# Optimization experiments

Hardware: AMD Instinct MI355X
Metric: run time of the kernel (lower is better)

Reference implementation:

```python
import jax, jax.numpy as jnp
import numpy as np

B, S, D, H = 4, 1024, 1024, 16
DH = D // H  # head dim = 64
NEG = 1e9  # keras Softmax masking constant for fp32


def setup_inputs() -> dict:
    key = jax.random.key(0)
    ks = jax.random.split(key, 7)
    return {
        "inputs": jax.random.normal(ks[0], (B, S, D), jnp.float32),
        "mask": jax.random.randint(ks[1], (B, 1, 1, S), 0, 2) > 0,
        "interaction": jax.random.normal(ks[2], (B, S, S, H), jnp.float32) * 0.1,
        "W_Q": jax.random.normal(ks[3], (D, D), jnp.float32) * 0.02,
        "W_K": jax.random.normal(ks[4], (D, D), jnp.float32) * 0.02,
        "W_V": jax.random.normal(ks[5], (D, D), jnp.float32) * 0.02,
        "W_O": jax.random.normal(ks[6], (D, D), jnp.float32) * 0.02,
    }


def reference(inputs, mask, interaction, W_Q, W_K, W_V, W_O):
    b, s, d = inputs.shape
    def proj(W):
        # [B,S,D] @ [D,D] -> [B,S,H,DH] -> [B,H,S,DH]
        return (inputs @ W).reshape(b, s, H, DH).transpose(0, 2, 1, 3)
    Q, K, V = proj(W_Q), proj(W_K), proj(W_V)
    scores = jnp.einsum("bhqd,bhkd->bhqk", Q, K) / (DH ** 0.5)
    # interaction [B,S,S,H] -> [B,H,S,S], additive bias before softmax
    scores = scores + interaction.transpose(0, 3, 1, 2)
    # keras Softmax(mask=...): add -1e9 where mask is False, softmax over last axis
    scores = jnp.where(mask, scores, scores - NEG)
    attn = jax.nn.softmax(scores, axis=-1)
    hidden = jnp.einsum("bhqk,bhkd->bhqd", attn, V)
    hidden = hidden.transpose(0, 2, 1, 3).reshape(b, s, d)
    return hidden @ W_O
```

## Files before the change

### kernel.cpp

```cpp
#include <hip/hip_runtime.h>
#include <hip/hip_bf16.h>
#include <stdint.h>

#define BDIM 4
#define SDIM 1024
#define DDIM 1024
#define HDIM 16
#define DHDIM 64

typedef __bf16 bf16_t;
typedef __bf16 bf16x8 __attribute__((ext_vector_type(8)));
typedef __bf16 bf16x4 __attribute__((ext_vector_type(4)));
typedef float f32x4 __attribute__((ext_vector_type(4)));

typedef __attribute__((address_space(3))) uint32_t lds_u32;
typedef const __attribute__((address_space(1))) uint32_t glb_u32;

__device__ __forceinline__ void glds16(const void* g, void* l) {
    __builtin_amdgcn_global_load_lds((glb_u32*)g, (lds_u32*)l, 16, 0, 0);
}


__global__ __launch_bounds__(256) void convert_x_kernel(const float* __restrict__ X,
                                                        bf16_t* __restrict__ Xb, int n) {
    int i = (blockIdx.x * 256 + threadIdx.x) * 4;
    if (i >= n) return;
    float4 v = *(const float4*)(X + i);
    bf16x4 o;
    o[0] = (bf16_t)v.x; o[1] = (bf16_t)v.y; o[2] = (bf16_t)v.z; o[3] = (bf16_t)v.w;
    *(bf16x4*)(Xb + i) = o;
}

__global__ __launch_bounds__(256) void transpose_w_kernel(const float* __restrict__ W0,
                                                          const float* __restrict__ W1,
                                                          const float* __restrict__ W2,
                                                          const float* __restrict__ W3,
                                                          bf16_t* __restrict__ Wt) {
    __shared__ float tile[32][33];
    int z = blockIdx.z;
    const float* W = (z == 0) ? W0 : (z == 1) ? W1 : (z == 2) ? W2 : W3;
    bf16_t* dst = Wt + (size_t)z * DDIM * DDIM;
    int bx = blockIdx.x * 32;
    int by = blockIdx.y * 32;
    int x = threadIdx.x & 31, y0 = threadIdx.x >> 5;
#pragma unroll
    for (int i = 0; i < 4; i++) {
        int y = y0 + i * 8;
        tile[y][x] = W[(size_t)(by + y) * DDIM + bx + x];
    }
    __syncthreads();
#pragma unroll
    for (int i = 0; i < 4; i++) {
        int y = y0 + i * 8;
        dst[(size_t)(bx + y) * DDIM + by + x] = (bf16_t)tile[x][y];
    }
}

__global__ __launch_bounds__(1024) void mask_flag_kernel(const unsigned char* __restrict__ mb,
                                                         int* __restrict__ flag) {
    __shared__ int any;
    if (threadIdx.x == 0) any = 0;
    __syncthreads();
    int loc = 0;
    for (int i = threadIdx.x; i < BDIM * SDIM; i += 1024)
        if ((i & 3) && mb[i]) loc = 1;
    if (loc) any = 1;
    __syncthreads();
    if (threadIdx.x == 0) *flag = any ? 1 : 0;
}

template <int MODE>
__global__ __launch_bounds__(256) void gemm_bt_kernel(const bf16_t* __restrict__ A,
                                                      const bf16_t* __restrict__ Bt,
                                                      bf16_t* __restrict__ Qo, bf16_t* __restrict__ Ko,
                                                      bf16_t* __restrict__ Vto, float* __restrict__ Co) {
    __shared__ bf16_t As[128 * 32];
    __shared__ bf16_t Bs[128 * 32];
    const int m0 = blockIdx.x * 128;
    const int n0 = blockIdx.y * 128;
    const int t = threadIdx.x;
    const int lane = t & 63, w = t >> 6;
    const int wm = w & 1, wn = w >> 1;
    const int low = lane & 15, quad = lane >> 4;
    f32x4 acc[4][4] = {};

    const int srow = w * 16 + (lane >> 2);
    const int koff = (lane & 3) * 8;
    const bf16_t* Ag = A + (size_t)(m0 + srow) * DDIM + koff;
    const bf16_t* Bg = Bt + (size_t)(n0 + srow) * DDIM + koff;
    bf16_t* AsW = As + w * 512;
    bf16_t* BsW = Bs + w * 512;

    for (int k0 = 0; k0 < DDIM; k0 += 32) {
        __syncthreads();
        glds16(Ag + k0, AsW);
        glds16(Ag + (size_t)64 * DDIM + k0, AsW + 64 * 32);
        glds16(Bg + k0, BsW);
        glds16(Bg + (size_t)64 * DDIM + k0, BsW + 64 * 32);
        __syncthreads();
        bf16x8 af[4], bv[4];
#pragma unroll
        for (int mt = 0; mt < 4; mt++)
            af[mt] = *(const bf16x8*)(As + (wm * 64 + mt * 16 + low) * 32 + quad * 8);
#pragma unroll
        for (int nt = 0; nt < 4; nt++)
            bv[nt] = *(const bf16x8*)(Bs + (wn * 64 + nt * 16 + low) * 32 + quad * 8);
#pragma unroll
        for (int mt = 0; mt < 4; mt++)
#pragma unroll
            for (int nt = 0; nt < 4; nt++)
                acc[mt][nt] = __builtin_amdgcn_mfma_f32_16x16x32_bf16(af[mt], bv[nt], acc[mt][nt], 0, 0, 0);
    }

#pragma unroll
    for (int mt = 0; mt < 4; mt++) {
        const int mbase = m0 + wm * 64 + mt * 16 + quad * 4;
#pragma unroll
        for (int nt = 0; nt < 4; nt++) {
            const int ncol = n0 + wn * 64 + nt * 16 + low;
            if (MODE == 0) {
                const int which = ncol >> 10, nl = ncol & 1023;
                const int hh = nl >> 6, dh = nl & 63;
                const int bb = mbase >> 10, s = mbase & 1023;
                if (which == 2) {
                    bf16x4 pv;
#pragma unroll
                    for (int r = 0; r < 4; r++) pv[r] = (bf16_t)acc[mt][nt][r];
                    *(bf16x4*)(Vto + ((size_t)((bb * HDIM + hh) * DHDIM + dh)) * SDIM + s) = pv;
                } else if (which == 0) {
#pragma unroll
                    for (int r = 0; r < 4; r++)
                        Qo[((size_t)(bb * HDIM + hh) * SDIM + (s + r)) * DHDIM + dh] =
                            (bf16_t)(acc[mt][nt][r] * 0.125f);
                } else {
#pragma unroll
                    for (int r = 0; r < 4; r++)
                        Ko[((size_t)(bb * HDIM + hh) * SDIM + (s + r)) * DHDIM + dh] =
                            (bf16_t)acc[mt][nt][r];
                }
            } else {
#pragma unroll
                for (int r = 0; r < 4; r++)
                    Co[(size_t)(mbase + r) * DDIM + ncol] = acc[mt][nt][r];
            }
        }
    }
}

__global__ __launch_bounds__(1024, 4) void attn_kernel(const bf16_t* __restrict__ Q,
                                                       const bf16_t* __restrict__ K,
                                                       const bf16_t* __restrict__ Vt,
                                                       const float* __restrict__ inter,
                                                       const unsigned char* __restrict__ maskb,
                                                       const int* __restrict__ flagp,
                                                       bf16_t* __restrict__ hid) {
    constexpr int KS = 40;
    constexpr int HS = 16 * KS + 8;
    __shared__ bf16_t bias_l[2][16 * HS];
    __shared__ bf16_t P[16][16 * KS];
    const int b = blockIdx.y;
    const int q0 = blockIdx.x * 16;
    const int t = threadIdx.x;
    const int w = t >> 6, lane = t & 63;
    const int low = lane & 15, quad = lane >> 4;
    const int h = w;
    const int mstride = (*flagp) ? 1 : 4;

    const int sh = lane & 15;
    const int sk0 = (lane >> 4) * 8;
    const float* srcB = inter + ((size_t)(b * SDIM + q0 + w) * SDIM + sk0) * HDIM + sh;
    const unsigned char* mb = maskb + (size_t)b * SDIM * mstride;
    const int stoff = sh * HS + w * KS + sk0;

    const bf16_t* Qb = Q + ((size_t)(b * HDIM + h) * SDIM + q0) * DHDIM;
    bf16x8 qf0 = *(const bf16x8*)(Qb + low * DHDIM + quad * 8);
    bf16x8 qf1 = *(const bf16x8*)(Qb + low * DHDIM + 32 + quad * 8);

    const bf16_t* Kb = K + (size_t)(b * HDIM + h) * SDIM * DHDIM;
    const bf16_t* VtB = Vt + (size_t)(b * HDIM + h) * DHDIM * SDIM;
    bf16_t* Pw = &P[w][0];

    float mrow = -3.0e38f, lrow = 0.f;
    f32x4 accO[4] = {};

    bf16x8 kA0 = *(const bf16x8*)(Kb + (size_t)(0 + low) * DHDIM + quad * 8);
    bf16x8 kA1 = *(const bf16x8*)(Kb + (size_t)(0 + low) * DHDIM + 32 + quad * 8);
    bf16x8 kB0 = *(const bf16x8*)(Kb + (size_t)(16 + low) * DHDIM + quad * 8);
    bf16x8 kB1 = *(const bf16x8*)(Kb + (size_t)(16 + low) * DHDIM + 32 + quad * 8);
    {
        float b0v[8], pen0[8];
#pragma unroll
        for (int j = 0; j < 8; j++) b0v[j] = srcB[j * HDIM];
        if (mstride == 1) {
            uint64_t mw = *(const uint64_t*)(mb + sk0);
#pragma unroll
            for (int j = 0; j < 8; j++) pen0[j] = ((mw >> (8 * j)) & 0xff) ? 0.f : 1.0e9f;
        } else {
            const int4* mp = (const int4*)(mb + (size_t)sk0 * 4);
            int4 ma = mp[0], mc = mp[1];
            pen0[0] = ma.x ? 0.f : 1.0e9f; pen0[1] = ma.y ? 0.f : 1.0e9f;
            pen0[2] = ma.z ? 0.f : 1.0e9f; pen0[3] = ma.w ? 0.f : 1.0e9f;
            pen0[4] = mc.x ? 0.f : 1.0e9f; pen0[5] = mc.y ? 0.f : 1.0e9f;
            pen0[6] = mc.z ? 0.f : 1.0e9f; pen0[7] = mc.w ? 0.f : 1.0e9f;
        }
        bf16x8 bw;
#pragma unroll
        for (int j = 0; j < 8; j++) bw[j] = (bf16_t)(b0v[j] - pen0[j]);
        *(bf16x8*)(&bias_l[0][stoff]) = bw;
    }

    for (int c = 0; c < SDIM / 32; c++) {
        __syncthreads();
        const int kbase = c * 32;

        bf16x8 vf[4];
#pragma unroll
        for (int nt = 0; nt < 4; nt++)
            vf[nt] = *(const bf16x8*)(VtB + (size_t)(nt * 16 + low) * SDIM + kbase + quad * 8);

        bf16x8 nA0, nA1, nB0, nB1;
        float nb[8], npen[8];
        if (c < SDIM / 32 - 1) {
            const int k2 = kbase + 32;
            const bf16_t* kpA = Kb + (size_t)(k2 + low) * DHDIM;
            const bf16_t* kpB = Kb + (size_t)(k2 + 16 + low) * DHDIM;
            nA0 = *(const bf16x8*)(kpA + quad * 8);
            nA1 = *(const bf16x8*)(kpA + 32 + quad * 8);
            nB0 = *(const bf16x8*)(kpB + quad * 8);
            nB1 = *(const bf16x8*)(kpB + 32 + quad * 8);
            const float* s2 = srcB + (size_t)(c + 1) * 512;
#pragma unroll
            for (int j = 0; j < 8; j++) nb[j] = s2[j * HDIM];
            const int kb2 = k2 + sk0;
            if (mstride == 1) {
                uint64_t mw = *(const uint64_t*)(mb + kb2);
#pragma unroll
                for (int j = 0; j < 8; j++) npen[j] = ((mw >> (8 * j)) & 0xff) ? 0.f : 1.0e9f;
            } else {
                const int4* mp = (const int4*)(mb + (size_t)kb2 * 4);
                int4 ma = mp[0], mc = mp[1];
                npen[0] = ma.x ? 0.f : 1.0e9f; npen[1] = ma.y ? 0.f : 1.0e9f;
                npen[2] = ma.z ? 0.f : 1.0e9f; npen[3] = ma.w ? 0.f : 1.0e9f;
                npen[4] = mc.x ? 0.f : 1.0e9f; npen[5] = mc.y ? 0.f : 1.0e9f;
                npen[6] = mc.z ? 0.f : 1.0e9f; npen[7] = mc.w ? 0.f : 1.0e9f;
            }
        }

        f32x4 s0 = {}, s1 = {};
        s0 = __builtin_amdgcn_mfma_f32_16x16x32_bf16(kA0, qf0, s0, 0, 0, 0);
        s0 = __builtin_amdgcn_mfma_f32_16x16x32_bf16(kA1, qf1, s0, 0, 0, 0);
        s1 = __builtin_amdgcn_mfma_f32_16x16x32_bf16(kB0, qf0, s1, 0, 0, 0);
        s1 = __builtin_amdgcn_mfma_f32_16x16x32_bf16(kB1, qf1, s1, 0, 0, 0);

        const bf16_t* bc = &bias_l[c & 1][h * HS + low * KS];
        bf16x4 bv0 = *(const bf16x4*)(bc + quad * 4);
        bf16x4 bv1 = *(const bf16x4*)(bc + 16 + quad * 4);
        float sv[8];
#pragma unroll
        for (int r = 0; r < 4; r++) {
            sv[r] = s0[r] + (float)bv0[r];
            sv[4 + r] = s1[r] + (float)bv1[r];
        }

        float vmx = sv[0];
#pragma unroll
        for (int j = 1; j < 8; j++) vmx = fmaxf(vmx, sv[j]);
        vmx = fmaxf(vmx, __shfl_xor(vmx, 16));
        vmx = fmaxf(vmx, __shfl_xor(vmx, 32));
        float mn = fmaxf(mrow, vmx);
        float alpha = __expf(mrow - mn);
        mrow = mn;
        float ps = 0.f;
        bf16x4 p0, p1;
#pragma unroll
        for (int j = 0; j < 4; j++) {
            float e0 = __expf(sv[j] - mn);
            float e1 = __expf(sv[4 + j] - mn);
            ps += e0 + e1;
            p0[j] = (bf16_t)e0;
            p1[j] = (bf16_t)e1;
        }
        ps += __shfl_xor(ps, 16);
        ps += __shfl_xor(ps, 32);
        lrow = lrow * alpha + ps;

#pragma unroll
        for (int r = 0; r < 4; r++) {
            float ar = __shfl(alpha, (lane & 48) | (quad * 4 + r));
#pragma unroll
            for (int nt = 0; nt < 4; nt++) accO[nt][r] *= ar;
        }

        *(bf16x4*)(Pw + low * KS + quad * 4) = p0;
        *(bf16x4*)(Pw + low * KS + 16 + quad * 4) = p1;
        bf16x8 pf = *(const bf16x8*)(Pw + low * KS + quad * 8);

#pragma unroll
        for (int nt = 0; nt < 4; nt++)
            accO[nt] = __builtin_amdgcn_mfma_f32_16x16x32_bf16(pf, vf[nt], accO[nt], 0, 0, 0);

        if (c < SDIM / 32 - 1) {
            bf16x8 bw;
#pragma unroll
            for (int j = 0; j < 8; j++) bw[j] = (bf16_t)(nb[j] - npen[j]);
            *(bf16x8*)(&bias_l[(c + 1) & 1][stoff]) = bw;
            kA0 = nA0; kA1 = nA1; kB0 = nB0; kB1 = nB1;
        }
    }

    float linv = 1.f / lrow;
#pragma unroll
    for (int r = 0; r < 4; r++) {
        float lr = __shfl(linv, (lane & 48) | (quad * 4 + r));
#pragma unroll
        for (int nt = 0; nt < 4; nt++) {
            hid[((size_t)b * SDIM + q0 + quad * 4 + r) * DDIM + h * 64 + nt * 16 + low] =
                (bf16_t)(accO[nt][r] * lr);
        }
    }
}


extern "C" void kernel_launch(void* const* d_in, const int* in_sizes, int n_in,
                              void* d_out, int out_size, void* d_ws, size_t ws_size,
                              hipStream_t stream) {
    const float* X = (const float*)d_in[0];
    const unsigned char* maskb = (const unsigned char*)d_in[1];
    const float* inter = (const float*)d_in[2];
    const float* WQ = (const float*)d_in[3];
    const float* WK = (const float*)d_in[4];
    const float* WV = (const float*)d_in[5];
    const float* WO = (const float*)d_in[6];
    float* out = (float*)d_out;

    char* ws = (char*)d_ws;
    const size_t MB = 1024 * 1024;
    bf16_t* Xb  = (bf16_t*)(ws + 0 * MB);
    bf16_t* Wt  = (bf16_t*)(ws + 8 * MB);
    bf16_t* Qm  = (bf16_t*)(ws + 16 * MB);
    bf16_t* Km  = (bf16_t*)(ws + 24 * MB);
    bf16_t* Vtm = (bf16_t*)(ws + 32 * MB);
    bf16_t* hid = (bf16_t*)(ws + 40 * MB);
    int* flag   = (int*)(ws + 48 * MB);

    convert_x_kernel<<<BDIM * SDIM * DDIM / (256 * 4), 256, 0, stream>>>(X, Xb, BDIM * SDIM * DDIM);
    transpose_w_kernel<<<dim3(32, 32, 4), 256, 0, stream>>>(WQ, WK, WV, WO, Wt);
    mask_flag_kernel<<<1, 1024, 0, stream>>>(maskb, flag);
    gemm_bt_kernel<0><<<dim3(32, 24), 256, 0, stream>>>(Xb, Wt, Qm, Km, Vtm, nullptr);
    attn_kernel<<<dim3(SDIM / 16, BDIM), 1024, 0, stream>>>(Qm, Km, Vtm, inter, maskb, flag, hid);
    gemm_bt_kernel<1><<<dim3(32, 8), 256, 0, stream>>>(hid, Wt + (size_t)3 * DDIM * DDIM,
                                                       nullptr, nullptr, nullptr, out);
}
```

Before: 543.0 us.

## Restructure attention blocks to 32 queries x 8 heads with XCD-aware mapping

The attention kernel now gives each block 32 query rows and half the heads (8 waves, 512 threads) instead of 16 rows and all 16 heads. Each K/V fragment is reused for two 16-row query tiles, and block IDs are mapped so blocks sharing a batch and head half land on the same XCD, which should improve L2 locality. The interaction bias is loaded as float4 vectors along the head axis with a scalar mask read, replacing strided scalar loads. The cost is that K prefetch into registers is dropped, the bias is written to LDS with scalar bf16 stores, the grid shrinks to 256 blocks, and register pressure rises from two sets of accumulators.

```diff
diff --git a/kernel.cpp b/kernel.cpp
--- a/kernel.cpp
+++ b/kernel.cpp
@@ -147,175 +147,212 @@
     }
 }
 
-__global__ __launch_bounds__(1024, 4) void attn_kernel(const bf16_t* __restrict__ Q,
-                                                       const bf16_t* __restrict__ K,
-                                                       const bf16_t* __restrict__ Vt,
-                                                       const float* __restrict__ inter,
-                                                       const unsigned char* __restrict__ maskb,
-                                                       const int* __restrict__ flagp,
-                                                       bf16_t* __restrict__ hid) {
+__global__ __launch_bounds__(512, 4) void attn_kernel(const bf16_t* __restrict__ Q,
+                                                      const bf16_t* __restrict__ K,
+                                                      const bf16_t* __restrict__ Vt,
+                                                      const float* __restrict__ inter,
+                                                      const unsigned char* __restrict__ maskb,
+                                                      const int* __restrict__ flagp,
+                                                      bf16_t* __restrict__ hid) {
     constexpr int KS = 40;
     constexpr int HS = 16 * KS + 8;
-    __shared__ bf16_t bias_l[2][16 * HS];
-    __shared__ bf16_t P[16][16 * KS];
-    const int b = blockIdx.y;
-    const int q0 = blockIdx.x * 16;
+    constexpr int BUFE = 2 * 8 * HS;
+    __shared__ bf16_t bias_l[2][BUFE];
+    __shared__ bf16_t P[8][16 * KS];
+    const int bid = blockIdx.x;
+    const int xcd = bid & 7;
+    const int b = xcd >> 1, hh = xcd & 1, qi = bid >> 3;
+    const int q0 = qi * 32;
     const int t = threadIdx.x;
     const int w = t >> 6, lane = t & 63;
     const int low = lane & 15, quad = lane >> 4;
-    const int h = w;
+    const int h = hh * 8 + w;
     const int mstride = (*flagp) ? 1 : 4;
 
-    const int sh = lane & 15;
-    const int sk0 = (lane >> 4) * 8;
-    const float* srcB = inter + ((size_t)(b * SDIM + q0 + w) * SDIM + sk0) * HDIM + sh;
+    const int sk = lane >> 1, shp = lane & 1;
+    const float* srcB = inter + ((size_t)(b * SDIM + q0) * SDIM + sk) * HDIM + hh * 8 + shp * 4;
     const unsigned char* mb = maskb + (size_t)b * SDIM * mstride;
-    const int stoff = sh * HS + w * KS + sk0;
+    constexpr size_t ROWSTRIDE = (size_t)SDIM * HDIM;
 
     const bf16_t* Qb = Q + ((size_t)(b * HDIM + h) * SDIM + q0) * DHDIM;
-    bf16x8 qf0 = *(const bf16x8*)(Qb + low * DHDIM + quad * 8);
-    bf16x8 qf1 = *(const bf16x8*)(Qb + low * DHDIM + 32 + quad * 8);
+    bf16x8 qa0 = *(const bf16x8*)(Qb + low * DHDIM + quad * 8);
+    bf16x8 qa1 = *(const bf16x8*)(Qb + low * DHDIM + 32 + quad * 8);
+    bf16x8 qb0 = *(const bf16x8*)(Qb + (16 + low) * DHDIM + quad * 8);
+    bf16x8 qb1 = *(const bf16x8*)(Qb + (16 + low) * DHDIM + 32 + quad * 8);
 
     const bf16_t* Kb = K + (size_t)(b * HDIM + h) * SDIM * DHDIM;
     const bf16_t* VtB = Vt + (size_t)(b * HDIM + h) * DHDIM * SDIM;
     bf16_t* Pw = &P[w][0];
 
-    float mrow = -3.0e38f, lrow = 0.f;
-    f32x4 accO[4] = {};
-
-    bf16x8 kA0 = *(const bf16x8*)(Kb + (size_t)(0 + low) * DHDIM + quad * 8);
-    bf16x8 kA1 = *(const bf16x8*)(Kb + (size_t)(0 + low) * DHDIM + 32 + quad * 8);
-    bf16x8 kB0 = *(const bf16x8*)(Kb + (size_t)(16 + low) * DHDIM + quad * 8);
-    bf16x8 kB1 = *(const bf16x8*)(Kb + (size_t)(16 + low) * DHDIM + 32 + quad * 8);
+    float mA = -3.0e38f, lA = 0.f, mB = -3.0e38f, lB = 0.f;
+    f32x4 accA[4] = {}, accB[4] = {};
+
     {
-        float b0v[8], pen0[8];
-#pragma unroll
-        for (int j = 0; j < 8; j++) b0v[j] = srcB[j * HDIM];
-        if (mstride == 1) {
-            uint64_t mw = *(const uint64_t*)(mb + sk0);
-#pragma unroll
-            for (int j = 0; j < 8; j++) pen0[j] = ((mw >> (8 * j)) & 0xff) ? 0.f : 1.0e9f;
-        } else {
-            const int4* mp = (const int4*)(mb + (size_t)sk0 * 4);
-            int4 ma = mp[0], mc = mp[1];
-            pen0[0] = ma.x ? 0.f : 1.0e9f; pen0[1] = ma.y ? 0.f : 1.0e9f;
-            pen0[2] = ma.z ? 0.f : 1.0e9f; pen0[3] = ma.w ? 0.f : 1.0e9f;
-            pen0[4] = mc.x ? 0.f : 1.0e9f; pen0[5] = mc.y ? 0.f : 1.0e9f;
-            pen0[6] = mc.z ? 0.f : 1.0e9f; pen0[7] = mc.w ? 0.f : 1.0e9f;
-        }
-        bf16x8 bw;
-#pragma unroll
-        for (int j = 0; j < 8; j++) bw[j] = (bf16_t)(b0v[j] - pen0[j]);
-        *(bf16x8*)(&bias_l[0][stoff]) = bw;
+        float4 v[4];
+#pragma unroll
+        for (int i = 0; i < 4; i++)
+            v[i] = *(const float4*)(srcB + (size_t)(w + i * 8) * ROWSTRIDE);
+        float pen = mb[sk * mstride] ? 0.f : 1.0e9f;
+#pragma unroll
+        for (int i = 0; i < 4; i++) {
+            const int r4 = w + i * 8;
+            bf16_t* d = &bias_l[0][(size_t)(r4 >> 4) * (8 * HS) + (shp * 4) * HS + (r4 & 15) * KS + sk];
+            d[0 * HS] = (bf16_t)(v[i].x - pen);
+            d[1 * HS] = (bf16_t)(v[i].y - pen);
+            d[2 * HS] = (bf16_t)(v[i].z - pen);
+            d[3 * HS] = (bf16_t)(v[i].w - pen);
+        }
     }
 
     for (int c = 0; c < SDIM / 32; c++) {
         __syncthreads();
         const int kbase = c * 32;
 
+        float4 nv[4]; float npen = 0.f;
+        if (c < SDIM / 32 - 1) {
+#pragma unroll
+            for (int i = 0; i < 4; i++)
+                nv[i] = *(const float4*)(srcB + (size_t)(w + i * 8) * ROWSTRIDE + (size_t)(c + 1) * 32 * HDIM);
+            npen = mb[((c + 1) * 32 + sk) * mstride] ? 0.f : 1.0e9f;
+        }
+
+        const bf16_t* kpA = Kb + (size_t)(kbase + low) * DHDIM;
+        const bf16_t* kpB = Kb + (size_t)(kbase + 16 + low) * DHDIM;
+        bf16x8 kA0 = *(const bf16x8*)(kpA + quad * 8);
+        bf16x8 kA1 = *(const bf16x8*)(kpA + 32 + quad * 8);
+        bf16x8 kB0 = *(const bf16x8*)(kpB + quad * 8);
+        bf16x8 kB1 = *(const bf16x8*)(kpB + 32 + quad * 8);
+
+        f32x4 sA0 = {}, sA1 = {}, sB0 = {}, sB1 = {};
+        sA0 = __builtin_amdgcn_mfma_f32_16x16x32_bf16(kA0, qa0, sA0, 0, 0, 0);
+        sA0 = __builtin_amdgcn_mfma_f32_16x16x32_bf16(kA1, qa1, sA0, 0, 0, 0);
+        sA1 = __builtin_amdgcn_mfma_f32_16x16x32_bf16(kB0, qa0, sA1, 0, 0, 0);
+        sA1 = __builtin_amdgcn_mfma_f32_16x16x32_bf16(kB1, qa1, sA1, 0, 0, 0);
+        sB0 = __builtin_amdgcn_mfma_f32_16x16x32_bf16(kA0, qb0, sB0, 0, 0, 0);
+        sB0 = __builtin_amdgcn_mfma_f32_16x16x32_bf16(kA1, qb1, sB0, 0, 0, 0);
+        sB1 = __builtin_amdgcn_mfma_f32_16x16x32_bf16(kB0, qb0, sB1, 0, 0, 0);
+        sB1 = __builtin_amdgcn_mfma_f32_16x16x32_bf16(kB1, qb1, sB1, 0, 0, 0);
+
         bf16x8 vf[4];
 #pragma unroll
         for (int nt = 0; nt < 4; nt++)
             vf[nt] = *(const bf16x8*)(VtB + (size_t)(nt * 16 + low) * SDIM + kbase + quad * 8);
 
-        bf16x8 nA0, nA1, nB0, nB1;
-        float nb[8], npen[8];
+        {
+            const bf16_t* bc = &bias_l[c & 1][(size_t)0 * (8 * HS) + w * HS + low * KS];
+            bf16x4 bv0 = *(const bf16x4*)(bc + quad * 4);
+            bf16x4 bv1 = *(const bf16x4*)(bc + 16 + quad * 4);
+            float sv[8];
+#pragma unroll
+            for (int r = 0; r < 4; r++) {
+                sv[r] = sA0[r] + (float)bv0[r];
+                sv[4 + r] = sA1[r] + (float)bv1[r];
+            }
+            float vmx = sv[0];
+#pragma unroll
+            for (int j = 1; j < 8; j++) vmx = fmaxf(vmx, sv[j]);
+            vmx = fmaxf(vmx, __shfl_xor(vmx, 16));
+            vmx = fmaxf(vmx, __shfl_xor(vmx, 32));
+            float mn = fmaxf(mA, vmx);
+            float alpha = __expf(mA - mn);
+            mA = mn;
+            float ps = 0.f;
+            bf16x4 p0, p1;
+#pragma unroll
+            for (int j = 0; j < 4; j++) {
+                float e0 = __expf(sv[j] - mn);
+                float e1 = __expf(sv[4 + j] - mn);
+                ps += e0 + e1;
+                p0[j] = (bf16_t)e0;
+                p1[j] = (bf16_t)e1;
+            }
+            ps += __shfl_xor(ps, 16);
+            ps += __shfl_xor(ps, 32);
+            lA = lA * alpha + ps;
+#pragma unroll
+            for (int r = 0; r < 4; r++) {
+                float ar = __shfl(alpha, (lane & 48) | (quad * 4 + r));
+#pragma unroll
+                for (int nt = 0; nt < 4; nt++) accA[nt][r] *= ar;
+            }
+            *(bf16x4*)(Pw + low * KS + quad * 4) = p0;
+            *(bf16x4*)(Pw + low * KS + 16 + quad * 4) = p1;
+            bf16x8 pf = *(const bf16x8*)(Pw + low * KS + quad * 8);
+#pragma unroll
+            for (int nt = 0; nt < 4; nt++)
+                accA[nt] = __builtin_amdgcn_mfma_f32_16x16x32_bf16(pf, vf[nt], accA[nt], 0, 0, 0);
+        }
+
+        {
+            const bf16_t* bc = &bias_l[c & 1][(size_t)1 * (8 * HS) + w * HS + low * KS];
+            bf16x4 bv0 = *(const bf16x4*)(bc + quad * 4);
+            bf16x4 bv1 = *(const bf16x4*)(bc + 16 + quad * 4);
+            float sv[8];
+#pragma unroll
+            for (int r = 0; r < 4; r++) {
+                sv[r] = sB0[r] + (float)bv0[r];
+                sv[4 + r] = sB1[r] + (float)bv1[r];
+            }
+            float vmx = sv[0];
+#pragma unroll
+            for (int j = 1; j < 8; j++) vmx = fmaxf(vmx, sv[j]);
+            vmx = fmaxf(vmx, __shfl_xor(vmx, 16));
+            vmx = fmaxf(vmx, __shfl_xor(vmx, 32));
+            float mn = fmaxf(mB, vmx);
+            float alpha = __expf(mB - mn);
+            mB = mn;
+            float ps = 0.f;
+            bf16x4 p0, p1;
+#pragma unroll
+            for (int j = 0; j < 4; j++) {
+                float e0 = __expf(sv[j] - mn);
+                float e1 = __expf(sv[4 + j] - mn);
+                ps += e0 + e1;
+                p0[j] = (bf16_t)e0;
+                p1[j] = (bf16_t)e1;
+            }
+            ps += __shfl_xor(ps, 16);
+            ps += __shfl_xor(ps, 32);
+            lB = lB * alpha + ps;
+#pragma unroll
+            for (int r = 0; r < 4; r++) {
+                float ar = __shfl(alpha, (lane & 48) | (quad * 4 + r));
+#pragma unroll
+                for (int nt = 0; nt < 4; nt++) accB[nt][r] *= ar;
+            }
+            *(bf16x4*)(Pw + low * KS + quad * 4) = p0;
+            *(bf16x4*)(Pw + low * KS + 16 + quad * 4) = p1;
+            bf16x8 pf = *(const bf16x8*)(Pw + low * KS + quad * 8);
+#pragma unroll
+            for (int nt = 0; nt < 4; nt++)
+                accB[nt] = __builtin_amdgcn_mfma_f32_16x16x32_bf16(pf, vf[nt], accB[nt], 0, 0, 0);
+        }
+
         if (c < SDIM / 32 - 1) {
-            const int k2 = kbase + 32;
-            const bf16_t* kpA = Kb + (size_t)(k2 + low) * DHDIM;
-            const bf16_t* kpB = Kb + (size_t)(k2 + 16 + low) * DHDIM;
-            nA0 = *(const bf16x8*)(kpA + quad * 8);
-            nA1 = *(const bf16x8*)(kpA + 32 + quad * 8);
-            nB0 = *(const bf16x8*)(kpB + quad * 8);
-            nB1 = *(const bf16x8*)(kpB + 32 + quad * 8);
-            const float* s2 = srcB + (size_t)(c + 1) * 512;
-#pragma unroll
-            for (int j = 0; j < 8; j++) nb[j] = s2[j * HDIM];
-            const int kb2 = k2 + sk0;
-            if (mstride == 1) {
-                uint64_t mw = *(const uint64_t*)(mb + kb2);
-#pragma unroll
-                for (int j = 0; j < 8; j++) npen[j] = ((mw >> (8 * j)) & 0xff) ? 0.f : 1.0e9f;
-            } else {
-                const int4* mp = (const int4*)(mb + (size_t)kb2 * 4);
-                int4 ma = mp[0], mc = mp[1];
-                npen[0] = ma.x ? 0.f : 1.0e9f; npen[1] = ma.y ? 0.f : 1.0e9f;
-                npen[2] = ma.z ? 0.f : 1.0e9f; npen[3] = ma.w ? 0.f : 1.0e9f;
-                npen[4] = mc.x ? 0.f : 1.0e9f; npen[5] = mc.y ? 0.f : 1.0e9f;
-                npen[6] = mc.z ? 0.f : 1.0e9f; npen[7] = mc.w ? 0.f : 1.0e9f;
-            }
-        }
-
-        f32x4 s0 = {}, s1 = {};
-        s0 = __builtin_amdgcn_mfma_f32_16x16x32_bf16(kA0, qf0, s0, 0, 0, 0);
-        s0 = __builtin_amdgcn_mfma_f32_16x16x32_bf16(kA1, qf1, s0, 0, 0, 0);
-        s1 = __builtin_amdgcn_mfma_f32_16x16x32_bf16(kB0, qf0, s1, 0, 0, 0);
-        s1 = __builtin_amdgcn_mfma_f32_16x16x32_bf16(kB1, qf1, s1, 0, 0, 0);
-
-        const bf16_t* bc = &bias_l[c & 1][h * HS + low * KS];
-        bf16x4 bv0 = *(const bf16x4*)(bc + quad * 4);
-        bf16x4 bv1 = *(const bf16x4*)(bc + 16 + quad * 4);
-        float sv[8];
-#pragma unroll
-        for (int r = 0; r < 4; r++) {
-            sv[r] = s0[r] + (float)bv0[r];
-            sv[4 + r] = s1[r] + (float)bv1[r];
-        }
-
-        float vmx = sv[0];
-#pragma unroll
-        for (int j = 1; j < 8; j++) vmx = fmaxf(vmx, sv[j]);
-        vmx = fmaxf(vmx, __shfl_xor(vmx, 16));
-        vmx = fmaxf(vmx, __shfl_xor(vmx, 32));
-        float mn = fmaxf(mrow, vmx);
-        float alpha = __expf(mrow - mn);
-        mrow = mn;
-        float ps = 0.f;
-        bf16x4 p0, p1;
-#pragma unroll
-        for (int j = 0; j < 4; j++) {
-            float e0 = __expf(sv[j] - mn);
-            float e1 = __expf(sv[4 + j] - mn);
-            ps += e0 + e1;
-            p0[j] = (bf16_t)e0;
-            p1[j] = (bf16_t)e1;
-        }
-        ps += __shfl_xor(ps, 16);
-        ps += __shfl_xor(ps, 32);
-        lrow = lrow * alpha + ps;
-
-#pragma unroll
-        for (int r = 0; r < 4; r++) {
-            float ar = __shfl(alpha, (lane & 48) | (quad * 4 + r));
-#pragma unroll
-            for (int nt = 0; nt < 4; nt++) accO[nt][r] *= ar;
-        }
-
-        *(bf16x4*)(Pw + low * KS + quad * 4) = p0;
-        *(bf16x4*)(Pw + low * KS + 16 + quad * 4) = p1;
-        bf16x8 pf = *(const bf16x8*)(Pw + low * KS + quad * 8);
-
-#pragma unroll
-        for (int nt = 0; nt < 4; nt++)
-            accO[nt] = __builtin_amdgcn_mfma_f32_16x16x32_bf16(pf, vf[nt], accO[nt], 0, 0, 0);
-
-        if (c < SDIM / 32 - 1) {
-            bf16x8 bw;
-#pragma unroll
-            for (int j = 0; j < 8; j++) bw[j] = (bf16_t)(nb[j] - npen[j]);
-            *(bf16x8*)(&bias_l[(c + 1) & 1][stoff]) = bw;
-            kA0 = nA0; kA1 = nA1; kB0 = nB0; kB1 = nB1;
-        }
-    }
-
-    float linv = 1.f / lrow;
+#pragma unroll
+            for (int i = 0; i < 4; i++) {
+                const int r4 = w + i * 8;
+                bf16_t* d = &bias_l[(c + 1) & 1]
+                                   [(size_t)(r4 >> 4) * (8 * HS) + (shp * 4) * HS + (r4 & 15) * KS + sk];
+                d[0 * HS] = (bf16_t)(nv[i].x - npen);
+                d[1 * HS] = (bf16_t)(nv[i].y - npen);
+                d[2 * HS] = (bf16_t)(nv[i].z - npen);
+                d[3 * HS] = (bf16_t)(nv[i].w - npen);
+            }
+        }
+    }
+
+    float liA = 1.f / lA, liB = 1.f / lB;
 #pragma unroll
     for (int r = 0; r < 4; r++) {
-        float lr = __shfl(linv, (lane & 48) | (quad * 4 + r));
+        float lrA = __shfl(liA, (lane & 48) | (quad * 4 + r));
+        float lrB = __shfl(liB, (lane & 48) | (quad * 4 + r));
 #pragma unroll
         for (int nt = 0; nt < 4; nt++) {
             hid[((size_t)b * SDIM + q0 + quad * 4 + r) * DDIM + h * 64 + nt * 16 + low] =
-                (bf16_t)(accO[nt][r] * lr);
+                (bf16_t)(accA[nt][r] * lrA);
+            hid[((size_t)b * SDIM + q0 + 16 + quad * 4 + r) * DDIM + h * 64 + nt * 16 + low] =
+                (bf16_t)(accB[nt][r] * lrB);
         }
     }
 }
@@ -347,7 +384,7 @@
     transpose_w_kernel<<<dim3(32, 32, 4), 256, 0, stream>>>(WQ, WK, WV, WO, Wt);
     mask_flag_kernel<<<1, 1024, 0, stream>>>(maskb, flag);
     gemm_bt_kernel<0><<<dim3(32, 24), 256, 0, stream>>>(Xb, Wt, Qm, Km, Vtm, nullptr);
-    attn_kernel<<<dim3(SDIM / 16, BDIM), 1024, 0, stream>>>(Qm, Km, Vtm, inter, maskb, flag, hid);
+    attn_kernel<<<dim3(256), 512, 0, stream>>>(Qm, Km, Vtm, inter, maskb, flag, hid);
     gemm_bt_kernel<1><<<dim3(32, 8), 256, 0, stream>>>(hid, Wt + (size_t)3 * DDIM * DDIM,
                                                        nullptr, nullptr, nullptr, out);
 }
```

Result: faster. 529.8 us (-2.4%).

## Split attention blocks per head-half with XCD-aware mapping and lazy softmax rescale

Applied to the files above, without the earlier changes.

The attention kernel now uses 512-thread blocks, each covering 8 heads instead of 16. Blocks are assigned through a 1D grid whose low bits pick the batch and head-half, so each XCD works on one (batch, head-half) pair and gets better L2 locality for K and V. The interaction bias is loaded with float4 reads along the head dimension and scattered into LDS as bf16. K fragments are no longer register-prefetched one chunk ahead. The online softmax skips rescaling unless the running max grows by more than 8, which cuts exp and multiply work but lets unnormalized values grow up to e^8 and adds a wave vote.

```diff
diff --git a/kernel.cpp b/kernel.cpp
--- a/kernel.cpp
+++ b/kernel.cpp
@@ -147,30 +147,31 @@
     }
 }
 
-__global__ __launch_bounds__(1024, 4) void attn_kernel(const bf16_t* __restrict__ Q,
-                                                       const bf16_t* __restrict__ K,
-                                                       const bf16_t* __restrict__ Vt,
-                                                       const float* __restrict__ inter,
-                                                       const unsigned char* __restrict__ maskb,
-                                                       const int* __restrict__ flagp,
-                                                       bf16_t* __restrict__ hid) {
+__global__ __launch_bounds__(512, 4) void attn_kernel(const bf16_t* __restrict__ Q,
+                                                      const bf16_t* __restrict__ K,
+                                                      const bf16_t* __restrict__ Vt,
+                                                      const float* __restrict__ inter,
+                                                      const unsigned char* __restrict__ maskb,
+                                                      const int* __restrict__ flagp,
+                                                      bf16_t* __restrict__ hid) {
     constexpr int KS = 40;
     constexpr int HS = 16 * KS + 8;
-    __shared__ bf16_t bias_l[2][16 * HS];
-    __shared__ bf16_t P[16][16 * KS];
-    const int b = blockIdx.y;
-    const int q0 = blockIdx.x * 16;
+    __shared__ bf16_t bias_l[2][8 * HS];
+    __shared__ bf16_t P[8][16 * KS];
+    const int bid = blockIdx.x;
+    const int xcd = bid & 7;
+    const int b = xcd >> 1, hh = xcd & 1;
+    const int q0 = (bid >> 3) * 16;
     const int t = threadIdx.x;
     const int w = t >> 6, lane = t & 63;
     const int low = lane & 15, quad = lane >> 4;
-    const int h = w;
+    const int h = hh * 8 + w;
     const int mstride = (*flagp) ? 1 : 4;
 
-    const int sh = lane & 15;
-    const int sk0 = (lane >> 4) * 8;
-    const float* srcB = inter + ((size_t)(b * SDIM + q0 + w) * SDIM + sk0) * HDIM + sh;
+    const int sk = lane >> 1, shp = lane & 1;
+    const float* srcB = inter + ((size_t)(b * SDIM + q0) * SDIM + sk) * HDIM + hh * 8 + shp * 4;
     const unsigned char* mb = maskb + (size_t)b * SDIM * mstride;
-    const int stoff = sh * HS + w * KS + sk0;
+    constexpr size_t ROWSTRIDE = (size_t)SDIM * HDIM;
 
     const bf16_t* Qb = Q + ((size_t)(b * HDIM + h) * SDIM + q0) * DHDIM;
     bf16x8 qf0 = *(const bf16x8*)(Qb + low * DHDIM + quad * 8);
@@ -183,67 +184,40 @@
     float mrow = -3.0e38f, lrow = 0.f;
     f32x4 accO[4] = {};
 
-    bf16x8 kA0 = *(const bf16x8*)(Kb + (size_t)(0 + low) * DHDIM + quad * 8);
-    bf16x8 kA1 = *(const bf16x8*)(Kb + (size_t)(0 + low) * DHDIM + 32 + quad * 8);
-    bf16x8 kB0 = *(const bf16x8*)(Kb + (size_t)(16 + low) * DHDIM + quad * 8);
-    bf16x8 kB1 = *(const bf16x8*)(Kb + (size_t)(16 + low) * DHDIM + 32 + quad * 8);
     {
-        float b0v[8], pen0[8];
-#pragma unroll
-        for (int j = 0; j < 8; j++) b0v[j] = srcB[j * HDIM];
-        if (mstride == 1) {
-            uint64_t mw = *(const uint64_t*)(mb + sk0);
-#pragma unroll
-            for (int j = 0; j < 8; j++) pen0[j] = ((mw >> (8 * j)) & 0xff) ? 0.f : 1.0e9f;
-        } else {
-            const int4* mp = (const int4*)(mb + (size_t)sk0 * 4);
-            int4 ma = mp[0], mc = mp[1];
-            pen0[0] = ma.x ? 0.f : 1.0e9f; pen0[1] = ma.y ? 0.f : 1.0e9f;
-            pen0[2] = ma.z ? 0.f : 1.0e9f; pen0[3] = ma.w ? 0.f : 1.0e9f;
-            pen0[4] = mc.x ? 0.f : 1.0e9f; pen0[5] = mc.y ? 0.f : 1.0e9f;
-            pen0[6] = mc.z ? 0.f : 1.0e9f; pen0[7] = mc.w ? 0.f : 1.0e9f;
-        }
-        bf16x8 bw;
-#pragma unroll
-        for (int j = 0; j < 8; j++) bw[j] = (bf16_t)(b0v[j] - pen0[j]);
-        *(bf16x8*)(&bias_l[0][stoff]) = bw;
+        float4 v0 = *(const float4*)(srcB + (size_t)w * ROWSTRIDE);
+        float4 v1 = *(const float4*)(srcB + (size_t)(w + 8) * ROWSTRIDE);
+        float pen = mb[sk * mstride] ? 0.f : 1.0e9f;
+        bf16_t* d0 = &bias_l[0][(shp * 4) * HS + w * KS + sk];
+        bf16_t* d1 = &bias_l[0][(shp * 4) * HS + (w + 8) * KS + sk];
+        d0[0 * HS] = (bf16_t)(v0.x - pen); d0[1 * HS] = (bf16_t)(v0.y - pen);
+        d0[2 * HS] = (bf16_t)(v0.z - pen); d0[3 * HS] = (bf16_t)(v0.w - pen);
+        d1[0 * HS] = (bf16_t)(v1.x - pen); d1[1 * HS] = (bf16_t)(v1.y - pen);
+        d1[2 * HS] = (bf16_t)(v1.z - pen); d1[3 * HS] = (bf16_t)(v1.w - pen);
     }
 
     for (int c = 0; c < SDIM / 32; c++) {
         __syncthreads();
         const int kbase = c * 32;
 
+        const bf16_t* kpA = Kb + (size_t)(kbase + low) * DHDIM;
+        const bf16_t* kpB = Kb + (size_t)(kbase + 16 + low) * DHDIM;
+        bf16x8 kA0 = *(const bf16x8*)(kpA + quad * 8);
+        bf16x8 kA1 = *(const bf16x8*)(kpA + 32 + quad * 8);
+        bf16x8 kB0 = *(const bf16x8*)(kpB + quad * 8);
+        bf16x8 kB1 = *(const bf16x8*)(kpB + 32 + quad * 8);
+
         bf16x8 vf[4];
 #pragma unroll
         for (int nt = 0; nt < 4; nt++)
             vf[nt] = *(const bf16x8*)(VtB + (size_t)(nt * 16 + low) * SDIM + kbase + quad * 8);
 
-        bf16x8 nA0, nA1, nB0, nB1;
-        float nb[8], npen[8];
+        float4 nv0, nv1; float npen = 0.f;
         if (c < SDIM / 32 - 1) {
-            const int k2 = kbase + 32;
-            const bf16_t* kpA = Kb + (size_t)(k2 + low) * DHDIM;
-            const bf16_t* kpB = Kb + (size_t)(k2 + 16 + low) * DHDIM;
-            nA0 = *(const bf16x8*)(kpA + quad * 8);
-            nA1 = *(const bf16x8*)(kpA + 32 + quad * 8);
-            nB0 = *(const bf16x8*)(kpB + quad * 8);
-            nB1 = *(const bf16x8*)(kpB + 32 + quad * 8);
-            const float* s2 = srcB + (size_t)(c + 1) * 512;
-#pragma unroll
-            for (int j = 0; j < 8; j++) nb[j] = s2[j * HDIM];
-            const int kb2 = k2 + sk0;
-            if (mstride == 1) {
-                uint64_t mw = *(const uint64_t*)(mb + kb2);
-#pragma unroll
-                for (int j = 0; j < 8; j++) npen[j] = ((mw >> (8 * j)) & 0xff) ? 0.f : 1.0e9f;
-            } else {
-                const int4* mp = (const int4*)(mb + (size_t)kb2 * 4);
-                int4 ma = mp[0], mc = mp[1];
-                npen[0] = ma.x ? 0.f : 1.0e9f; npen[1] = ma.y ? 0.f : 1.0e9f;
-                npen[2] = ma.z ? 0.f : 1.0e9f; npen[3] = ma.w ? 0.f : 1.0e9f;
-                npen[4] = mc.x ? 0.f : 1.0e9f; npen[5] = mc.y ? 0.f : 1.0e9f;
-                npen[6] = mc.z ? 0.f : 1.0e9f; npen[7] = mc.w ? 0.f : 1.0e9f;
-            }
+            const float* s2 = srcB + (size_t)(c + 1) * 32 * HDIM;
+            nv0 = *(const float4*)(s2 + (size_t)w * ROWSTRIDE);
+            nv1 = *(const float4*)(s2 + (size_t)(w + 8) * ROWSTRIDE);
+            npen = mb[((c + 1) * 32 + sk) * mstride] ? 0.f : 1.0e9f;
         }
 
         f32x4 s0 = {}, s1 = {};
@@ -252,7 +226,7 @@
         s1 = __builtin_amdgcn_mfma_f32_16x16x32_bf16(kB0, qf0, s1, 0, 0, 0);
         s1 = __builtin_amdgcn_mfma_f32_16x16x32_bf16(kB1, qf1, s1, 0, 0, 0);
 
-        const bf16_t* bc = &bias_l[c & 1][h * HS + low * KS];
+        const bf16_t* bc = &bias_l[c & 1][w * HS + low * KS];
         bf16x4 bv0 = *(const bf16x4*)(bc + quad * 4);
         bf16x4 bv1 = *(const bf16x4*)(bc + 16 + quad * 4);
         float sv[8];
@@ -262,34 +236,32 @@
             sv[4 + r] = s1[r] + (float)bv1[r];
         }
 
-        float vmx = sv[0];
-#pragma unroll
-        for (int j = 1; j < 8; j++) vmx = fmaxf(vmx, sv[j]);
+        float vmx = fmaxf(fmaxf(fmaxf(sv[0], sv[1]), fmaxf(sv[2], sv[3])),
+                          fmaxf(fmaxf(sv[4], sv[5]), fmaxf(sv[6], sv[7])));
         vmx = fmaxf(vmx, __shfl_xor(vmx, 16));
         vmx = fmaxf(vmx, __shfl_xor(vmx, 32));
-        float mn = fmaxf(mrow, vmx);
-        float alpha = __expf(mrow - mn);
-        mrow = mn;
-        float ps = 0.f;
+        if (__any(vmx > mrow + 8.f)) {
+            float mn = fmaxf(mrow, vmx);
+            float alpha = __expf(mrow - mn);
+            mrow = mn;
+            lrow *= alpha;
+#pragma unroll
+            for (int r = 0; r < 4; r++) {
+                float ar = __shfl(alpha, (lane & 48) | (quad * 4 + r));
+#pragma unroll
+                for (int nt = 0; nt < 4; nt++) accO[nt][r] *= ar;
+            }
+        }
+        float e[8];
+#pragma unroll
+        for (int j = 0; j < 8; j++) e[j] = __expf(sv[j] - mrow);
         bf16x4 p0, p1;
 #pragma unroll
-        for (int j = 0; j < 4; j++) {
-            float e0 = __expf(sv[j] - mn);
-            float e1 = __expf(sv[4 + j] - mn);
-            ps += e0 + e1;
-            p0[j] = (bf16_t)e0;
-            p1[j] = (bf16_t)e1;
-        }
+        for (int j = 0; j < 4; j++) { p0[j] = (bf16_t)e[j]; p1[j] = (bf16_t)e[4 + j]; }
+        float ps = ((e[0] + e[1]) + (e[2] + e[3])) + ((e[4] + e[5]) + (e[6] + e[7]));
         ps += __shfl_xor(ps, 16);
         ps += __shfl_xor(ps, 32);
-        lrow = lrow * alpha + ps;
-
-#pragma unroll
-        for (int r = 0; r < 4; r++) {
-            float ar = __shfl(alpha, (lane & 48) | (quad * 4 + r));
-#pragma unroll
-            for (int nt = 0; nt < 4; nt++) accO[nt][r] *= ar;
-        }
+        lrow += ps;
 
         *(bf16x4*)(Pw + low * KS + quad * 4) = p0;
         *(bf16x4*)(Pw + low * KS + 16 + quad * 4) = p1;
@@ -300,11 +272,12 @@
             accO[nt] = __builtin_amdgcn_mfma_f32_16x16x32_bf16(pf, vf[nt], accO[nt], 0, 0, 0);
 
         if (c < SDIM / 32 - 1) {
-            bf16x8 bw;
-#pragma unroll
-            for (int j = 0; j < 8; j++) bw[j] = (bf16_t)(nb[j] - npen[j]);
-            *(bf16x8*)(&bias_l[(c + 1) & 1][stoff]) = bw;
-            kA0 = nA0; kA1 = nA1; kB0 = nB0; kB1 = nB1;
+            bf16_t* d0 = &bias_l[(c + 1) & 1][(shp * 4) * HS + w * KS + sk];
+            bf16_t* d1 = &bias_l[(c + 1) & 1][(shp * 4) * HS + (w + 8) * KS + sk];
+            d0[0 * HS] = (bf16_t)(nv0.x - npen); d0[1 * HS] = (bf16_t)(nv0.y - npen);
+            d0[2 * HS] = (bf16_t)(nv0.z - npen); d0[3 * HS] = (bf16_t)(nv0.w - npen);
+            d1[0 * HS] = (bf16_t)(nv1.x - npen); d1[1 * HS] = (bf16_t)(nv1.y - npen);
+            d1[2 * HS] = (bf16_t)(nv1.z - npen); d1[3 * HS] = (bf16_t)(nv1.w - npen);
         }
     }
 
@@ -347,7 +320,7 @@
     transpose_w_kernel<<<dim3(32, 32, 4), 256, 0, stream>>>(WQ, WK, WV, WO, Wt);
     mask_flag_kernel<<<1, 1024, 0, stream>>>(maskb, flag);
     gemm_bt_kernel<0><<<dim3(32, 24), 256, 0, stream>>>(Xb, Wt, Qm, Km, Vtm, nullptr);
-    attn_kernel<<<dim3(SDIM / 16, BDIM), 1024, 0, stream>>>(Qm, Km, Vtm, inter, maskb, flag, hid);
+    attn_kernel<<<dim3(512), 512, 0, stream>>>(Qm, Km, Vtm, inter, maskb, flag, hid);
     gemm_bt_kernel<1><<<dim3(32, 8), 256, 0, stream>>>(hid, Wt + (size_t)3 * DDIM * DDIM,
                                                        nullptr, nullptr, nullptr, out);
 }
```

New measurement: 550.1 us. No clear change (+1.3%).
